# Optimization experiments

Hardware: AMD Instinct MI355X
Metric: run time of the kernel (lower is better)

Reference implementation:

```python
import jax, jax.numpy as jnp
import numpy as np

N_NODES = 100000
N_EDGES = 625000
D_IN = 128
D_HID = 256


def setup_inputs() -> dict:
    key = jax.random.key(0)
    ks = jax.random.split(key, 9)
    x = jax.random.normal(ks[0], (N_NODES, D_IN), dtype=jnp.float32)
    edge_index = jax.random.randint(ks[1], (2, N_EDGES), 0, N_NODES, dtype=jnp.int64)
    s = 1.0 / np.sqrt(D_IN)
    # SAGEConv params: lin_l applied to mean-aggregated neighbors (with bias),
    # lin_r applied to root features (no bias) -- PyG defaults.
    w_l = jax.random.uniform(ks[2], (D_IN, D_HID), minval=-s, maxval=s, dtype=jnp.float32)
    b_l = jax.random.uniform(ks[3], (D_HID,), minval=-s, maxval=s, dtype=jnp.float32)
    w_r = jax.random.uniform(ks[4], (D_IN, D_HID), minval=-s, maxval=s, dtype=jnp.float32)
    sh = 1.0 / np.sqrt(D_HID)
    w_p = jax.random.uniform(ks[5], (D_HID, 7), minval=-sh, maxval=sh, dtype=jnp.float32)
    b_p = jax.random.uniform(ks[6], (7,), minval=-sh, maxval=sh, dtype=jnp.float32)
    w_s = jax.random.uniform(ks[7], (D_HID, 6), minval=-sh, maxval=sh, dtype=jnp.float32)
    b_s = jax.random.uniform(ks[8], (6,), minval=-sh, maxval=sh, dtype=jnp.float32)
    return {"x": x, "edge_index": edge_index, "w_l": w_l, "b_l": b_l, "w_r": w_r,
            "w_p": w_p, "b_p": b_p, "w_s": w_s, "b_s": b_s}


def reference(x, edge_index, w_l, b_l, w_r, w_p, b_p, w_s, b_s):
    src, dst = edge_index[0], edge_index[1]
    n = x.shape[0]
    # SAGEConv mean aggregation: mean of source-node features over each target
    agg = jax.ops.segment_sum(x[src], dst, num_segments=n)          # [N, D_IN]
    cnt = jax.ops.segment_sum(jnp.ones(src.shape, x.dtype), dst, num_segments=n)
    mean = agg / jnp.maximum(cnt, 1.0)[:, None]                      # isolated nodes -> 0
    h = mean @ w_l + b_l + x @ w_r                                   # [N, D_HID]
    h = jax.nn.relu(h)                                               # dropout = identity (eval)
    pr = h @ w_p + b_p                                               # [N, 7]
    sv = h @ w_s + b_s                                               # [N, 6]
    return jax.nn.log_softmax(pr, axis=1), jax.nn.log_softmax(sv, axis=1)
```

## Files before the change

### kernel.cpp

```cpp
#include <hip/hip_runtime.h>
#include <hip/hip_bf16.h>
#include <math.h>

#define NN 100000
#define NE 625000
#define DIN 128
#define DH 256
#define NROWS 100096
#define CAP 32

#define HS_STRIDE 264
#define MEAN_STRIDE 136

#define EDGE_BLOCKS  2442
#define XCAST_BLOCKS 12500
#define PACKW_BLOCKS 32
#define PACKH_BLOCKS 2
#define PREP_BLOCKS  (EDGE_BLOCKS + XCAST_BLOCKS + PACKW_BLOCKS + PACKH_BLOCKS)

typedef __attribute__((ext_vector_type(8))) short bf16x8;
typedef __attribute__((ext_vector_type(4))) float f32x4;
typedef __attribute__((ext_vector_type(4))) unsigned int u32x4;

__device__ __forceinline__ unsigned short f2bf(float f) {
    unsigned u = __builtin_bit_cast(unsigned, f);
    u += 0x7fffu + ((u >> 16) & 1u);
    return (unsigned short)(u >> 16);
}
__device__ __forceinline__ float bflo(unsigned u) {
    return __builtin_bit_cast(float, u << 16);
}
__device__ __forceinline__ float bfhi(unsigned u) {
    return __builtin_bit_cast(float, u & 0xffff0000u);
}

__device__ __forceinline__ void gll16(const unsigned short* g, unsigned short* l) {
    __builtin_amdgcn_global_load_lds(
        (const __attribute__((address_space(1))) unsigned int*)(const void*)g,
        (__attribute__((address_space(3))) unsigned int*)(void*)l, 16, 0, 0);
}

__global__ __launch_bounds__(256)
void prep(const float* __restrict__ x, const int* __restrict__ ei,
          const float* __restrict__ w_l, const float* __restrict__ w_r,
          const float* __restrict__ w_p, const float* __restrict__ w_s,
          const float* __restrict__ b_p, const float* __restrict__ b_s,
          unsigned short* __restrict__ X, unsigned short* __restrict__ Bp,
          unsigned short* __restrict__ whp, float* __restrict__ bhc,
          int* __restrict__ deg, int* __restrict__ elist) {
    const int b = blockIdx.x;
    const int t = threadIdx.x;

    if (b < EDGE_BLOCKS) {
        int e = b * 256 + t;
        if (e < NE) {
            int dst = ei[NE + e];
            int src = ei[e];
            int pos = atomicAdd(&deg[dst], 1);
            if (pos < CAP)
                __builtin_nontemporal_store(src, elist + dst * CAP + pos);
        }
    } else if (b < EDGE_BLOCKS + XCAST_BLOCKS) {
        int idx = (b - EDGE_BLOCKS) * 256 + t;
        int n = idx >> 5;
        int j4 = (idx & 31) * 4;
        float4 v = *reinterpret_cast<const float4*>(x + (size_t)n * DIN + j4);
        ushort4 o = { f2bf(v.x), f2bf(v.y), f2bf(v.z), f2bf(v.w) };
        *reinterpret_cast<ushort4*>(X + (size_t)n * 128 + j4) = o;
    } else if (b < EDGE_BLOCKS + XCAST_BLOCKS + PACKW_BLOCKS) {
        int tid = (b - EDGE_BLOCKS - XCAST_BLOCKS) * 256 + t;
        int kt = tid >> 10;
        int ct = (tid >> 6) & 15;
        int L = tid & 63;
        int k0 = kt * 32 + (L >> 4) * 8;
        int c = ct * 16 + (L & 15);
        unsigned short v[8];
#pragma unroll
        for (int j = 0; j < 8; ++j) {
            int k = k0 + j;
            float w = (k < 128) ? w_l[k * 256 + c] : w_r[(k - 128) * 256 + c];
            v[j] = f2bf(w);
        }
        int g = ((ct >> 3) << 6) + (kt << 3) + (ct & 7);
        *reinterpret_cast<bf16x8*>(Bp + (size_t)(g * 64 + L) * 8) =
            *reinterpret_cast<const bf16x8*>(v);
    } else {
        int tid = (b - EDGE_BLOCKS - XCAST_BLOCKS - PACKW_BLOCKS) * 256 + t;
        int kt = tid >> 6;
        int L = tid & 63;
        int k0 = kt * 32 + (L >> 4) * 8;
        int c = L & 15;
        unsigned short v[8];
#pragma unroll
        for (int j = 0; j < 8; ++j) {
            int k = k0 + j;
            float w = (c < 7) ? w_p[k * 7 + c] : (c < 13 ? w_s[k * 6 + (c - 7)] : 0.f);
            v[j] = f2bf(w);
        }
        *reinterpret_cast<bf16x8*>(whp + (size_t)tid * 8) =
            *reinterpret_cast<const bf16x8*>(v);
        if (tid < 16)
            bhc[tid] = (tid < 7) ? b_p[tid] : (tid < 13 ? b_s[tid - 7] : 0.f);
        if (tid >= 16 && tid < 32) {
            uint4 z = {0u, 0u, 0u, 0u};
            *reinterpret_cast<uint4*>(X + (size_t)NN * 128 + (tid - 16) * 8) = z;
        }
    }
}

__device__ __forceinline__ void gacc8(float* m, const uint4& v) {
    m[0] += bflo(v.x); m[1] += bfhi(v.x);
    m[2] += bflo(v.y); m[3] += bfhi(v.y);
    m[4] += bflo(v.z); m[5] += bfhi(v.z);
    m[6] += bflo(v.w); m[7] += bfhi(v.w);
}

__global__ __launch_bounds__(512, 4)
void sage_fused(const unsigned short* __restrict__ X,
                const unsigned short* __restrict__ Bp,
                const float* __restrict__ b_l,
                const unsigned short* __restrict__ whp,
                const float* __restrict__ bhc,
                const int* __restrict__ elist,
                const int* __restrict__ deg,
                float* __restrict__ out) {
    __shared__ __align__(16) unsigned char smem[76288];
    unsigned short* Bs = (unsigned short*)smem;
    unsigned short* mean_lds = (unsigned short*)smem;
    unsigned short* hs = (unsigned short*)smem;
    float* o13 = (float*)(smem + 67584);

    const int t = threadIdx.x;
    const int wave = t >> 6;
    const int L = t & 63;
    const int q = L >> 4;
    const int m15 = L & 15;
    const int node0 = blockIdx.x * 128;
    const int node = node0 + wave * 16 + m15;

    for (int p = 0; p < 2; ++p) {
        const int rl = p * 64 + (t >> 3);
        const int n = node0 + rl;
        const int h = t & 7;
        const int d = (n < NN) ? deg[n] : 0;
        const int dl = (d < CAP) ? d : CAP;
        const int dpad = (dl + 1) & ~1;
        const int base = (n < NN ? n : 0) * CAP;

        float macc[16];
#pragma unroll
        for (int j = 0; j < 16; ++j) macc[j] = 0.f;

        int s0 = elist[base + 0];
        int s1 = elist[base + 1];
        s0 = (dl > 0) ? s0 : NN;
        s1 = (dl > 1) ? s1 : NN;

        for (int i = 0; i < dpad; i += 2) {
            const unsigned short* xr0 = X + (size_t)s0 * 128 + h * 16;
            const unsigned short* xr1 = X + (size_t)s1 * 128 + h * 16;
            uint4 a0 = *reinterpret_cast<const uint4*>(xr0);
            uint4 a1 = *reinterpret_cast<const uint4*>(xr0 + 8);
            uint4 b0 = *reinterpret_cast<const uint4*>(xr1);
            uint4 b1 = *reinterpret_cast<const uint4*>(xr1 + 8);
            const int i2 = i + 2;
            int t0 = elist[base + (i2 & 31)];
            int t1 = elist[base + ((i2 + 1) & 31)];
            t0 = (i2 < dl) ? t0 : NN;
            t1 = (i2 + 1 < dl) ? t1 : NN;
            gacc8(macc, a0);
            gacc8(macc + 8, a1);
            gacc8(macc, b0);
            gacc8(macc + 8, b1);
            s0 = t0; s1 = t1;
        }

        const float invd = (dl > 0) ? 1.f / (float)dl : 0.f;
        u32x4 w0, w1;
#pragma unroll
        for (int j = 0; j < 4; ++j) {
            unsigned lo = f2bf(macc[2 * j] * invd);
            unsigned hi = f2bf(macc[2 * j + 1] * invd);
            w0[j] = lo | (hi << 16);
            unsigned lo2 = f2bf(macc[8 + 2 * j] * invd);
            unsigned hi2 = f2bf(macc[8 + 2 * j + 1] * invd);
            w1[j] = lo2 | (hi2 << 16);
        }
        unsigned short* mrow = mean_lds + rl * MEAN_STRIDE + h * 16;
        *reinterpret_cast<u32x4*>(mrow) = w0;
        *reinterpret_cast<u32x4*>(mrow + 8) = w1;
    }

    __syncthreads();

    bf16x8 afrag[8];
    {
        const unsigned short* mrow = mean_lds + (size_t)(wave * 16 + m15) * MEAN_STRIDE;
#pragma unroll
        for (int kt = 0; kt < 4; ++kt)
            afrag[kt] = *reinterpret_cast<const bf16x8*>(mrow + kt * 32 + q * 8);
        const unsigned short* xrow = X + (size_t)node * 128;
#pragma unroll
        for (int kt = 4; kt < 8; ++kt)
            afrag[kt] = *reinterpret_cast<const bf16x8*>(xrow + (kt - 4) * 32 + q * 8);
    }

    f32x4 acc[16];
#pragma unroll
    for (int ct = 0; ct < 16; ++ct) acc[ct] = (f32x4){0.f, 0.f, 0.f, 0.f};

    __syncthreads();

#pragma unroll
    for (int rr = 0; rr < 8; ++rr)
        gll16(Bp + (size_t)(rr * 512 + t) * 8,
              Bs + (size_t)(rr * 512 + (wave << 6)) * 8);

    __syncthreads();

#pragma unroll
    for (int kt = 0; kt < 8; ++kt) {
#pragma unroll
        for (int c7 = 0; c7 < 8; ++c7) {
            bf16x8 b = *reinterpret_cast<const bf16x8*>(
                Bs + ((size_t)(kt * 8 + c7) * 64 + L) * 8);
            acc[c7] = __builtin_amdgcn_mfma_f32_16x16x32_bf16(afrag[kt], b, acc[c7], 0, 0, 0);
        }
    }

    __syncthreads();

#pragma unroll
    for (int rr = 0; rr < 8; ++rr)
        gll16(Bp + 32768 + (size_t)(rr * 512 + t) * 8,
              Bs + (size_t)(rr * 512 + (wave << 6)) * 8);
    __syncthreads();

#pragma unroll
    for (int kt = 0; kt < 8; ++kt) {
#pragma unroll
        for (int c7 = 0; c7 < 8; ++c7) {
            bf16x8 b = *reinterpret_cast<const bf16x8*>(
                Bs + ((size_t)(kt * 8 + c7) * 64 + L) * 8);
            acc[8 + c7] = __builtin_amdgcn_mfma_f32_16x16x32_bf16(afrag[kt], b, acc[8 + c7], 0, 0, 0);
        }
    }

    __syncthreads();

#pragma unroll
    for (int ct = 0; ct < 16; ++ct) {
        const int c = ct * 16 + m15;
        const float blv = b_l[c];
        const int r0 = wave * 16 + q * 4;
#pragma unroll
        for (int rr = 0; rr < 4; ++rr)
            hs[(r0 + rr) * HS_STRIDE + c] = f2bf(fmaxf(acc[ct][rr] + blv, 0.f));
    }
    __syncthreads();

    {
        f32x4 acch = (f32x4){0.f, 0.f, 0.f, 0.f};
        const unsigned short* hrow = hs + (size_t)(wave * 16 + m15) * HS_STRIDE;
#pragma unroll
        for (int kt = 0; kt < 8; ++kt) {
            bf16x8 ah = *reinterpret_cast<const bf16x8*>(hrow + kt * 32 + q * 8);
            bf16x8 bh = *reinterpret_cast<const bf16x8*>(whp + ((size_t)(kt * 64 + L)) * 8);
            acch = __builtin_amdgcn_mfma_f32_16x16x32_bf16(ah, bh, acch, 0, 0, 0);
        }
        if (m15 < 13) {
            const float bh = bhc[m15];
#pragma unroll
            for (int rr = 0; rr < 4; ++rr)
                o13[(wave * 16 + q * 4 + rr) * 17 + m15] = acch[rr] + bh;
        }
    }
    __syncthreads();

    if (t < 128) {
        const int gnode = node0 + t;
        if (gnode < NN) {
            float v[7], mx = -1e30f;
#pragma unroll
            for (int j = 0; j < 7; ++j) { v[j] = o13[t * 17 + j]; mx = fmaxf(mx, v[j]); }
            float sum = 0.f;
#pragma unroll
            for (int j = 0; j < 7; ++j) sum += expf(v[j] - mx);
            const float lse = mx + logf(sum);
#pragma unroll
            for (int j = 0; j < 7; ++j) out[(size_t)gnode * 7 + j] = v[j] - lse;

            float u[6], mx2 = -1e30f;
#pragma unroll
            for (int j = 0; j < 6; ++j) { u[j] = o13[t * 17 + 7 + j]; mx2 = fmaxf(mx2, u[j]); }
            float sum2 = 0.f;
#pragma unroll
            for (int j = 0; j < 6; ++j) sum2 += expf(u[j] - mx2);
            const float lse2 = mx2 + logf(sum2);
#pragma unroll
            for (int j = 0; j < 6; ++j) out[(size_t)NN * 7 + (size_t)gnode * 6 + j] = u[j] - lse2;
        }
    }
}

extern "C" void kernel_launch(void* const* d_in, const int* in_sizes, int n_in,
                              void* d_out, int out_size, void* d_ws, size_t ws_size,
                              hipStream_t stream) {
    const float* x   = (const float*)d_in[0];
    const int*   ei  = (const int*)d_in[1];
    const float* w_l = (const float*)d_in[2];
    const float* b_l = (const float*)d_in[3];
    const float* w_r = (const float*)d_in[4];
    const float* w_p = (const float*)d_in[5];
    const float* b_p = (const float*)d_in[6];
    const float* w_s = (const float*)d_in[7];
    const float* b_s = (const float*)d_in[8];
    float* out = (float*)d_out;

    unsigned short* X   = (unsigned short*)d_ws;
    unsigned short* Bp  = X + (size_t)NROWS * 128;
    unsigned short* whp = Bp + 65536;
    float* bhc  = (float*)(whp + 4096);
    int* deg    = (int*)(bhc + 16);
    int* elist  = deg + NN;

    hipMemsetAsync(deg, 0, NN * sizeof(int), stream);

    prep<<<PREP_BLOCKS, 256, 0, stream>>>(x, ei, w_l, w_r, w_p, w_s, b_p, b_s,
                                          X, Bp, whp, bhc, deg, elist);

    sage_fused<<<NROWS / 128, 512, 0, stream>>>(X, Bp, b_l, whp, bhc,
                                                elist, deg, out);
}
```

Measured before the change: 197.5 us.

## Fuse memset, prep and main kernel into one cooperative persistent kernel

Replaces the memset plus two launches with one cooperative kernel of 512 persistent blocks. Two grid-wide barriers separate degree zeroing, prep and the tiled SAGE compute. Blocks loop over virtual prep blocks and node tiles. The aim is to remove launch gaps and kernel boundaries, at the cost of grid-sync overhead, fixed occupancy during prep, and lost overlap from the persistent loop. If the cooperative launch fails, it falls back to the original three-step sequence.

```diff
diff --git a/kernel.cpp b/kernel.cpp
--- a/kernel.cpp
+++ b/kernel.cpp
@@ -1,6 +1,9 @@
 #include <hip/hip_runtime.h>
+#include <hip/hip_cooperative_groups.h>
 #include <hip/hip_bf16.h>
 #include <math.h>
+
+namespace cg = cooperative_groups;
 
 #define NN 100000
 #define NE 625000
@@ -12,11 +15,14 @@
 #define HS_STRIDE 264
 #define MEAN_STRIDE 136
 
-#define EDGE_BLOCKS  2442
-#define XCAST_BLOCKS 12500
-#define PACKW_BLOCKS 32
-#define PACKH_BLOCKS 2
-#define PREP_BLOCKS  (EDGE_BLOCKS + XCAST_BLOCKS + PACKW_BLOCKS + PACKH_BLOCKS)
+#define GRIDB 512
+#define NTILES (NROWS / 128)
+
+#define EDGE_VB  1221
+#define XCAST_VB 6250
+#define PACKW_VB 16
+#define PACKH_VB 1
+#define PREP_VB  (EDGE_VB + XCAST_VB + PACKW_VB + PACKH_VB)
 
 typedef __attribute__((ext_vector_type(8))) short bf16x8;
 typedef __attribute__((ext_vector_type(4))) float f32x4;
@@ -40,19 +46,24 @@
         (__attribute__((address_space(3))) unsigned int*)(void*)l, 16, 0, 0);
 }
 
-__global__ __launch_bounds__(256)
-void prep(const float* __restrict__ x, const int* __restrict__ ei,
-          const float* __restrict__ w_l, const float* __restrict__ w_r,
-          const float* __restrict__ w_p, const float* __restrict__ w_s,
-          const float* __restrict__ b_p, const float* __restrict__ b_s,
-          unsigned short* __restrict__ X, unsigned short* __restrict__ Bp,
-          unsigned short* __restrict__ whp, float* __restrict__ bhc,
-          int* __restrict__ deg, int* __restrict__ elist) {
-    const int b = blockIdx.x;
-    const int t = threadIdx.x;
-
-    if (b < EDGE_BLOCKS) {
-        int e = b * 256 + t;
+__device__ __forceinline__ void gacc8(float* m, const uint4& v) {
+    m[0] += bflo(v.x); m[1] += bfhi(v.x);
+    m[2] += bflo(v.y); m[3] += bfhi(v.y);
+    m[4] += bflo(v.z); m[5] += bfhi(v.z);
+    m[6] += bflo(v.w); m[7] += bfhi(v.w);
+}
+
+__device__ __forceinline__ void prep_body(
+        int vb, int t,
+        const float* __restrict__ x, const int* __restrict__ ei,
+        const float* __restrict__ w_l, const float* __restrict__ w_r,
+        const float* __restrict__ w_p, const float* __restrict__ w_s,
+        const float* __restrict__ b_p, const float* __restrict__ b_s,
+        unsigned short* __restrict__ X, unsigned short* __restrict__ Bp,
+        unsigned short* __restrict__ whp, float* __restrict__ bhc,
+        int* __restrict__ deg, int* __restrict__ elist) {
+    if (vb < EDGE_VB) {
+        int e = vb * 512 + t;
         if (e < NE) {
             int dst = ei[NE + e];
             int src = ei[e];
@@ -60,15 +71,15 @@
             if (pos < CAP)
                 __builtin_nontemporal_store(src, elist + dst * CAP + pos);
         }
-    } else if (b < EDGE_BLOCKS + XCAST_BLOCKS) {
-        int idx = (b - EDGE_BLOCKS) * 256 + t;
+    } else if (vb < EDGE_VB + XCAST_VB) {
+        int idx = (vb - EDGE_VB) * 512 + t;
         int n = idx >> 5;
         int j4 = (idx & 31) * 4;
         float4 v = *reinterpret_cast<const float4*>(x + (size_t)n * DIN + j4);
         ushort4 o = { f2bf(v.x), f2bf(v.y), f2bf(v.z), f2bf(v.w) };
         *reinterpret_cast<ushort4*>(X + (size_t)n * 128 + j4) = o;
-    } else if (b < EDGE_BLOCKS + XCAST_BLOCKS + PACKW_BLOCKS) {
-        int tid = (b - EDGE_BLOCKS - XCAST_BLOCKS) * 256 + t;
+    } else if (vb < EDGE_VB + XCAST_VB + PACKW_VB) {
+        int tid = (vb - EDGE_VB - XCAST_VB) * 512 + t;
         int kt = tid >> 10;
         int ct = (tid >> 6) & 15;
         int L = tid & 63;
@@ -85,7 +96,7 @@
         *reinterpret_cast<bf16x8*>(Bp + (size_t)(g * 64 + L) * 8) =
             *reinterpret_cast<const bf16x8*>(v);
     } else {
-        int tid = (b - EDGE_BLOCKS - XCAST_BLOCKS - PACKW_BLOCKS) * 256 + t;
+        int tid = t;
         int kt = tid >> 6;
         int L = tid & 63;
         int k0 = kt * 32 + (L >> 4) * 8;
@@ -108,34 +119,25 @@
     }
 }
 
-__device__ __forceinline__ void gacc8(float* m, const uint4& v) {
-    m[0] += bflo(v.x); m[1] += bfhi(v.x);
-    m[2] += bflo(v.y); m[3] += bfhi(v.y);
-    m[4] += bflo(v.z); m[5] += bfhi(v.z);
-    m[6] += bflo(v.w); m[7] += bfhi(v.w);
-}
-
-__global__ __launch_bounds__(512, 4)
-void sage_fused(const unsigned short* __restrict__ X,
-                const unsigned short* __restrict__ Bp,
-                const float* __restrict__ b_l,
-                const unsigned short* __restrict__ whp,
-                const float* __restrict__ bhc,
-                const int* __restrict__ elist,
-                const int* __restrict__ deg,
-                float* __restrict__ out) {
-    __shared__ __align__(16) unsigned char smem[76288];
+__device__ __forceinline__ void tile_body(
+        int node0, int t, unsigned char* smem,
+        const unsigned short* __restrict__ X,
+        const unsigned short* __restrict__ Bp,
+        const float* __restrict__ b_l,
+        const unsigned short* __restrict__ whp,
+        const float* __restrict__ bhc,
+        const int* __restrict__ elist,
+        const int* __restrict__ deg,
+        float* __restrict__ out) {
     unsigned short* Bs = (unsigned short*)smem;
     unsigned short* mean_lds = (unsigned short*)smem;
     unsigned short* hs = (unsigned short*)smem;
     float* o13 = (float*)(smem + 67584);
 
-    const int t = threadIdx.x;
     const int wave = t >> 6;
     const int L = t & 63;
     const int q = L >> 4;
     const int m15 = L & 15;
-    const int node0 = blockIdx.x * 128;
     const int node = node0 + wave * 16 + m15;
 
     for (int p = 0; p < 2; ++p) {
@@ -301,6 +303,62 @@
             for (int j = 0; j < 6; ++j) out[(size_t)NN * 7 + (size_t)gnode * 6 + j] = u[j] - lse2;
         }
     }
+    __syncthreads();
+}
+
+__global__ __launch_bounds__(512, 4)
+void sage_mega(const float* __restrict__ x, const int* __restrict__ ei,
+               const float* __restrict__ w_l, const float* __restrict__ b_l,
+               const float* __restrict__ w_r, const float* __restrict__ w_p,
+               const float* __restrict__ b_p, const float* __restrict__ w_s,
+               const float* __restrict__ b_s,
+               unsigned short* __restrict__ X, unsigned short* __restrict__ Bp,
+               unsigned short* __restrict__ whp, float* __restrict__ bhc,
+               int* __restrict__ deg, int* __restrict__ elist,
+               float* __restrict__ out) {
+    __shared__ __align__(16) unsigned char smem[76288];
+    cg::grid_group grid = cg::this_grid();
+    const int t = threadIdx.x;
+
+    for (int i = blockIdx.x * 512 + t; i < NN; i += GRIDB * 512)
+        atomicExch(&deg[i], 0);
+
+    grid.sync();
+
+    for (int vb = blockIdx.x; vb < PREP_VB; vb += GRIDB)
+        prep_body(vb, t, x, ei, w_l, w_r, w_p, w_s, b_p, b_s,
+                  X, Bp, whp, bhc, deg, elist);
+
+    grid.sync();
+
+    for (int tile = blockIdx.x; tile < NTILES; tile += GRIDB)
+        tile_body(tile * 128, t, smem, X, Bp, b_l, whp, bhc, elist, deg, out);
+}
+
+__global__ __launch_bounds__(512)
+void prep_fb(const float* __restrict__ x, const int* __restrict__ ei,
+             const float* __restrict__ w_l, const float* __restrict__ w_r,
+             const float* __restrict__ w_p, const float* __restrict__ w_s,
+             const float* __restrict__ b_p, const float* __restrict__ b_s,
+             unsigned short* __restrict__ X, unsigned short* __restrict__ Bp,
+             unsigned short* __restrict__ whp, float* __restrict__ bhc,
+             int* __restrict__ deg, int* __restrict__ elist) {
+    prep_body(blockIdx.x, threadIdx.x, x, ei, w_l, w_r, w_p, w_s, b_p, b_s,
+              X, Bp, whp, bhc, deg, elist);
+}
+
+__global__ __launch_bounds__(512, 4)
+void fused_fb(const unsigned short* __restrict__ X,
+              const unsigned short* __restrict__ Bp,
+              const float* __restrict__ b_l,
+              const unsigned short* __restrict__ whp,
+              const float* __restrict__ bhc,
+              const int* __restrict__ elist,
+              const int* __restrict__ deg,
+              float* __restrict__ out) {
+    __shared__ __align__(16) unsigned char smem[76288];
+    tile_body(blockIdx.x * 128, threadIdx.x, smem,
+              X, Bp, b_l, whp, bhc, elist, deg, out);
 }
 
 extern "C" void kernel_launch(void* const* d_in, const int* in_sizes, int n_in,
@@ -324,11 +382,19 @@
     int* deg    = (int*)(bhc + 16);
     int* elist  = deg + NN;
 
-    hipMemsetAsync(deg, 0, NN * sizeof(int), stream);
-
-    prep<<<PREP_BLOCKS, 256, 0, stream>>>(x, ei, w_l, w_r, w_p, w_s, b_p, b_s,
-                                          X, Bp, whp, bhc, deg, elist);
-
-    sage_fused<<<NROWS / 128, 512, 0, stream>>>(X, Bp, b_l, whp, bhc,
-                                                elist, deg, out);
-}
+    void* kargs[] = { (void*)&x, (void*)&ei, (void*)&w_l, (void*)&b_l,
+                      (void*)&w_r, (void*)&w_p, (void*)&b_p, (void*)&w_s,
+                      (void*)&b_s, (void*)&X, (void*)&Bp, (void*)&whp,
+                      (void*)&bhc, (void*)&deg, (void*)&elist, (void*)&out };
+
+    hipError_t err = hipLaunchCooperativeKernel(
+        (const void*)sage_mega, dim3(GRIDB), dim3(512), kargs, 0, stream);
+
+    if (err != hipSuccess) {
+        hipMemsetAsync(deg, 0, NN * sizeof(int), stream);
+        prep_fb<<<PREP_VB, 512, 0, stream>>>(x, ei, w_l, w_r, w_p, w_s, b_p, b_s,
+                                             X, Bp, whp, bhc, deg, elist);
+        fused_fb<<<NTILES, 512, 0, stream>>>(X, Bp, b_l, whp, bhc,
+                                             elist, deg, out);
+    }
+}
```

After: 344.6 us. 1.75x slower.

## Shrink LDS footprint by streaming weights in quarters and splitting h staging

Applied to the files above, without the earlier changes.

The fused SAGE kernel now loads the packed layer weights into LDS in four 16 KB quarter tiles instead of two 32 KB halves, with the weight packing layout changed to match. The hidden-activation staging buffer is halved, so waves 0-3 and then waves 4-7 take turns writing h and running the head MFMA. Together these cut shared memory from about 76 KB to 42 KB, and launch bounds are raised to target 6 blocks per CU. The aim is higher occupancy to hide gather latency, at the cost of extra barriers and serialised head computation between the two wave halves.

```diff
diff --git a/kernel.cpp b/kernel.cpp
--- a/kernel.cpp
+++ b/kernel.cpp
@@ -38,6 +38,13 @@
     __builtin_amdgcn_global_load_lds(
         (const __attribute__((address_space(1))) unsigned int*)(const void*)g,
         (__attribute__((address_space(3))) unsigned int*)(void*)l, 16, 0, 0);
+}
+
+__device__ __forceinline__ void gacc8(float* m, const uint4& v) {
+    m[0] += bflo(v.x); m[1] += bfhi(v.x);
+    m[2] += bflo(v.y); m[3] += bfhi(v.y);
+    m[4] += bflo(v.z); m[5] += bfhi(v.z);
+    m[6] += bflo(v.w); m[7] += bfhi(v.w);
 }
 
 __global__ __launch_bounds__(256)
@@ -81,7 +88,7 @@
             float w = (k < 128) ? w_l[k * 256 + c] : w_r[(k - 128) * 256 + c];
             v[j] = f2bf(w);
         }
-        int g = ((ct >> 3) << 6) + (kt << 3) + (ct & 7);
+        int g = ((ct >> 2) << 5) + (kt << 2) + (ct & 3);
         *reinterpret_cast<bf16x8*>(Bp + (size_t)(g * 64 + L) * 8) =
             *reinterpret_cast<const bf16x8*>(v);
     } else {
@@ -108,14 +115,7 @@
     }
 }
 
-__device__ __forceinline__ void gacc8(float* m, const uint4& v) {
-    m[0] += bflo(v.x); m[1] += bfhi(v.x);
-    m[2] += bflo(v.y); m[3] += bfhi(v.y);
-    m[4] += bflo(v.z); m[5] += bfhi(v.z);
-    m[6] += bflo(v.w); m[7] += bfhi(v.w);
-}
-
-__global__ __launch_bounds__(512, 4)
+__global__ __launch_bounds__(512, 6)
 void sage_fused(const unsigned short* __restrict__ X,
                 const unsigned short* __restrict__ Bp,
                 const float* __restrict__ b_l,
@@ -124,11 +124,11 @@
                 const int* __restrict__ elist,
                 const int* __restrict__ deg,
                 float* __restrict__ out) {
-    __shared__ __align__(16) unsigned char smem[76288];
+    __shared__ __align__(16) unsigned char smem[42496];
     unsigned short* Bs = (unsigned short*)smem;
     unsigned short* mean_lds = (unsigned short*)smem;
-    unsigned short* hs = (unsigned short*)smem;
-    float* o13 = (float*)(smem + 67584);
+    unsigned short* hs_half = (unsigned short*)smem;
+    float* o13 = (float*)(smem + 33792);
 
     const int t = threadIdx.x;
     const int wave = t >> 6;
@@ -212,56 +212,66 @@
     __syncthreads();
 
 #pragma unroll
-    for (int rr = 0; rr < 8; ++rr)
-        gll16(Bp + (size_t)(rr * 512 + t) * 8,
-              Bs + (size_t)(rr * 512 + (wave << 6)) * 8);
-
+    for (int qd = 0; qd < 4; ++qd) {
+#pragma unroll
+        for (int rr = 0; rr < 4; ++rr)
+            gll16(Bp + (size_t)(qd * 16384) + (size_t)(rr * 512 + t) * 8,
+                  Bs + (size_t)(rr * 512 + (wave << 6)) * 8);
+        __syncthreads();
+#pragma unroll
+        for (int kt = 0; kt < 8; ++kt) {
+#pragma unroll
+            for (int c2 = 0; c2 < 4; ++c2) {
+                bf16x8 b = *reinterpret_cast<const bf16x8*>(
+                    Bs + ((size_t)((kt << 2) + c2) * 64 + L) * 8);
+                acc[qd * 4 + c2] = __builtin_amdgcn_mfma_f32_16x16x32_bf16(
+                    afrag[kt], b, acc[qd * 4 + c2], 0, 0, 0);
+            }
+        }
+        __syncthreads();
+    }
+
+    if (wave < 4) {
+        const int lr0 = wave * 16 + q * 4;
+#pragma unroll
+        for (int ct = 0; ct < 16; ++ct) {
+            const int c = ct * 16 + m15;
+            const float blv = b_l[c];
+#pragma unroll
+            for (int rr = 0; rr < 4; ++rr)
+                hs_half[(lr0 + rr) * HS_STRIDE + c] =
+                    f2bf(fmaxf(acc[ct][rr] + blv, 0.f));
+        }
+        f32x4 acch = (f32x4){0.f, 0.f, 0.f, 0.f};
+        const unsigned short* hrow = hs_half + (size_t)(wave * 16 + m15) * HS_STRIDE;
+#pragma unroll
+        for (int kt = 0; kt < 8; ++kt) {
+            bf16x8 ah = *reinterpret_cast<const bf16x8*>(hrow + kt * 32 + q * 8);
+            bf16x8 bh = *reinterpret_cast<const bf16x8*>(whp + ((size_t)(kt * 64 + L)) * 8);
+            acch = __builtin_amdgcn_mfma_f32_16x16x32_bf16(ah, bh, acch, 0, 0, 0);
+        }
+        if (m15 < 13) {
+            const float bh = bhc[m15];
+#pragma unroll
+            for (int rr = 0; rr < 4; ++rr)
+                o13[(wave * 16 + q * 4 + rr) * 17 + m15] = acch[rr] + bh;
+        }
+    }
     __syncthreads();
 
-#pragma unroll
-    for (int kt = 0; kt < 8; ++kt) {
-#pragma unroll
-        for (int c7 = 0; c7 < 8; ++c7) {
-            bf16x8 b = *reinterpret_cast<const bf16x8*>(
-                Bs + ((size_t)(kt * 8 + c7) * 64 + L) * 8);
-            acc[c7] = __builtin_amdgcn_mfma_f32_16x16x32_bf16(afrag[kt], b, acc[c7], 0, 0, 0);
-        }
-    }
-
-    __syncthreads();
-
-#pragma unroll
-    for (int rr = 0; rr < 8; ++rr)
-        gll16(Bp + 32768 + (size_t)(rr * 512 + t) * 8,
-              Bs + (size_t)(rr * 512 + (wave << 6)) * 8);
-    __syncthreads();
-
-#pragma unroll
-    for (int kt = 0; kt < 8; ++kt) {
-#pragma unroll
-        for (int c7 = 0; c7 < 8; ++c7) {
-            bf16x8 b = *reinterpret_cast<const bf16x8*>(
-                Bs + ((size_t)(kt * 8 + c7) * 64 + L) * 8);
-            acc[8 + c7] = __builtin_amdgcn_mfma_f32_16x16x32_bf16(afrag[kt], b, acc[8 + c7], 0, 0, 0);
-        }
-    }
-
-    __syncthreads();
-
-#pragma unroll
-    for (int ct = 0; ct < 16; ++ct) {
-        const int c = ct * 16 + m15;
-        const float blv = b_l[c];
-        const int r0 = wave * 16 + q * 4;
-#pragma unroll
-        for (int rr = 0; rr < 4; ++rr)
-            hs[(r0 + rr) * HS_STRIDE + c] = f2bf(fmaxf(acc[ct][rr] + blv, 0.f));
-    }
-    __syncthreads();
-
-    {
+    if (wave >= 4) {
+        const int lr0 = (wave - 4) * 16 + q * 4;
+#pragma unroll
+        for (int ct = 0; ct < 16; ++ct) {
+            const int c = ct * 16 + m15;
+            const float blv = b_l[c];
+#pragma unroll
+            for (int rr = 0; rr < 4; ++rr)
+                hs_half[(lr0 + rr) * HS_STRIDE + c] =
+                    f2bf(fmaxf(acc[ct][rr] + blv, 0.f));
+        }
         f32x4 acch = (f32x4){0.f, 0.f, 0.f, 0.f};
-        const unsigned short* hrow = hs + (size_t)(wave * 16 + m15) * HS_STRIDE;
+        const unsigned short* hrow = hs_half + (size_t)((wave - 4) * 16 + m15) * HS_STRIDE;
 #pragma unroll
         for (int kt = 0; kt < 8; ++kt) {
             bf16x8 ah = *reinterpret_cast<const bf16x8*>(hrow + kt * 32 + q * 8);
```

Result: slower. 208.9 us (+5.8%).
